# Kernel tuning notes

Hardware: AMD Instinct MI355X
Metric: run time of the kernel (lower is better)

Reference implementation:

```python
import jax, jax.numpy as jnp
import numpy as np

N = 50000
E = 600000
C = 128          # out_channels (== in_channels)
L = 3            # num_conv layers
HID = 32
NUM_CLASSES = 7


def setup_inputs() -> dict:
    key = jax.random.key(0)
    ks = jax.random.split(key, 16)
    bound = 1.0 / np.sqrt(C)
    inp = {
        "x": jax.random.normal(ks[0], (N, C), dtype=jnp.float32),
        "edge_index": jax.random.randint(ks[1], (2, E), 0, N, dtype=jnp.int32),
        "edge_weight": jax.random.uniform(ks[2], (E,), dtype=jnp.float32),
        # GatedGraphConv weight: [num_layers, C, C], uniform(-1/sqrt(C), 1/sqrt(C))
        "conv_weight": jax.random.uniform(ks[3], (L, C, C), minval=-bound, maxval=bound, dtype=jnp.float32),
        # GRUCell params (torch layout: [3C, C] for ih and hh, gate order r,z,n)
        "w_ih": jax.random.uniform(ks[4], (3 * C, C), minval=-bound, maxval=bound, dtype=jnp.float32),
        "w_hh": jax.random.uniform(ks[5], (3 * C, C), minval=-bound, maxval=bound, dtype=jnp.float32),
        "b_ih": jax.random.uniform(ks[6], (3 * C,), minval=-bound, maxval=bound, dtype=jnp.float32),
        "b_hh": jax.random.uniform(ks[7], (3 * C,), minval=-bound, maxval=bound, dtype=jnp.float32),
        # MLP: C -> 32 -> 32 -> 32 -> NUM_CLASSES, tanh between hidden layers
        "w0": jax.random.normal(ks[8], (HID, C), dtype=jnp.float32) * 0.05,
        "b0": jnp.zeros((HID,), dtype=jnp.float32),
        "w1": jax.random.normal(ks[9], (HID, HID), dtype=jnp.float32) * 0.1,
        "b1": jnp.zeros((HID,), dtype=jnp.float32),
        "w2": jax.random.normal(ks[10], (HID, HID), dtype=jnp.float32) * 0.1,
        "b2": jnp.zeros((HID,), dtype=jnp.float32),
        "w3": jax.random.normal(ks[11], (NUM_CLASSES, HID), dtype=jnp.float32) * 0.1,
        "b3": jnp.zeros((NUM_CLASSES,), dtype=jnp.float32),
    }
    return inp


def _gru_cell(m, h, w_ih, w_hh, b_ih, b_hh):
    # torch GRUCell: gates ordered (r, z, n)
    gx = m @ w_ih.T + b_ih          # [N, 3C]
    gh = h @ w_hh.T + b_hh          # [N, 3C]
    xr, xz, xn = jnp.split(gx, 3, axis=-1)
    hr, hz, hn = jnp.split(gh, 3, axis=-1)
    r = jax.nn.sigmoid(xr + hr)
    z = jax.nn.sigmoid(xz + hz)
    n = jnp.tanh(xn + r * hn)
    return (1.0 - z) * n + z * h


def reference(x, edge_index, edge_weight, conv_weight, w_ih, w_hh, b_ih, b_hh,
              w0, b0, w1, b1, w2, b2, w3, b3):
    src, dst = edge_index[0], edge_index[1]
    h = x  # in_channels == out_channels, no padding needed
    for i in range(L):
        m = h @ conv_weight[i]                          # [N, C] dense GEMM
        msgs = edge_weight[:, None] * m[src]            # gather + edge weighting [E, C]
        agg = jax.ops.segment_sum(msgs, dst, num_segments=N)  # scatter-add [N, C]
        h = _gru_cell(agg, h, w_ih, w_hh, b_ih, b_hh)
    # MLP with tanh between hidden layers, linear last
    y = jnp.tanh(h @ w0.T + b0)
    y = jnp.tanh(y @ w1.T + b1)
    y = jnp.tanh(y @ w2.T + b2)
    y = y @ w3.T + b3
    return jax.nn.log_softmax(y, axis=-1)
```

## Files before the change

### kernel.cpp

```cpp
#include <hip/hip_runtime.h>
#include <hip/hip_bf16.h>
#include <math.h>

#define NN 50000
#define NE 600000
#define CC 128
#define NL 3
#define NRG (NN / 16)
#define C_RG 4
#define G_RG 4
#define SCAN_B 196

typedef __attribute__((ext_vector_type(8))) short bf16x8;
typedef __attribute__((ext_vector_type(4))) float f32x4;
typedef unsigned short ushort_t;
typedef unsigned int uint_t;

__device__ inline ushort_t f2bf(float f) {
    __hip_bfloat16 b = __float2bfloat16(f);
    return *reinterpret_cast<ushort_t*>(&b);
}
__device__ inline float bf2f(ushort_t u) {
    return __uint_as_float(((uint_t)u) << 16);
}
__device__ inline float fsig(float x) {
    return __builtin_amdgcn_rcpf(1.f + __builtin_amdgcn_exp2f(-1.44269504f * x));
}
__device__ inline float ftanh(float x) {
    float e = __builtin_amdgcn_exp2f(2.88539008f * fabsf(x));
    float t = 1.f - 2.f * __builtin_amdgcn_rcpf(e + 1.f);
    return copysignf(t, x);
}

__global__ __launch_bounds__(256) void k_cvt(const float* __restrict__ x,
                                             ushort_t* __restrict__ h_bf) {
    size_t i = (size_t)blockIdx.x * 256 + threadIdx.x;
    float4 v = ((const float4*)x)[i];
    ushort4 u;
    u.x = f2bf(v.x); u.y = f2bf(v.y); u.z = f2bf(v.z); u.w = f2bf(v.w);
    ((ushort4*)h_bf)[i] = u;
}

__global__ __launch_bounds__(256) void k_wpack(const float* __restrict__ W,
                                               ushort_t* __restrict__ pk) {
    int tid = blockIdx.x * 256 + threadIdx.x;
    int e = tid & 7;
    int l = (tid >> 3) & 63;
    int s = (tid >> 9) & 3;
    int rest = tid >> 11;
    int g = rest % 3, c0 = rest / 3;
    int row = g * 128 + c0 * 16 + (l & 15);
    int col = s * 32 + (l >> 4) * 8 + e;
    pk[tid] = f2bf(W[row * 128 + col]);
}

__global__ __launch_bounds__(256) void k_cpack(const float* __restrict__ cw,
                                               ushort_t* __restrict__ pk) {
    int tid = blockIdx.x * 256 + threadIdx.x;
    int e = tid & 7;
    int l = (tid >> 3) & 63;
    int s = (tid >> 9) & 3;
    int rest = tid >> 11;
    int c0 = rest & 7, layer = rest >> 3;
    int c = c0 * 16 + (l & 15);
    int k = s * 32 + (l >> 4) * 8 + e;
    pk[tid] = f2bf(cw[layer * 16384 + k * 128 + c]);
}

__global__ __launch_bounds__(256) void k_mpack(const float* __restrict__ w0,
                                               const float* __restrict__ w1,
                                               const float* __restrict__ w2,
                                               const float* __restrict__ w3,
                                               ushort_t* __restrict__ pk) {
    int tid = blockIdx.x * 256 + threadIdx.x;
    if (tid >= 6656) return;
    int e = tid & 7;
    int l = (tid >> 3) & 63;
    int lr = l & 15, lg = l >> 4;
    if (tid < 4096) {
        int s = (tid >> 9) & 3;
        int c0 = tid >> 11;
        pk[tid] = f2bf(w0[(c0 * 16 + lr) * 128 + s * 32 + lg * 8 + e]);
    } else if (tid < 5120) {
        int c0 = (tid - 4096) >> 9;
        pk[tid] = f2bf(w1[(c0 * 16 + lr) * 32 + lg * 8 + e]);
    } else if (tid < 6144) {
        int c0 = (tid - 5120) >> 9;
        pk[tid] = f2bf(w2[(c0 * 16 + lr) * 32 + lg * 8 + e]);
    } else {
        pk[tid] = (lr < 7) ? f2bf(w3[lr * 32 + lg * 8 + e]) : (ushort_t)0;
    }
}

__global__ __launch_bounds__(256) void k_count(const int* __restrict__ dst,
                                               int* __restrict__ deg) {
    int e = blockIdx.x * 256 + threadIdx.x;
    if (e < NE) atomicAdd(&deg[dst[e]], 1);
}

__global__ __launch_bounds__(256) void k_scan1(const int* __restrict__ deg,
                                               int* __restrict__ off,
                                               int* __restrict__ bsum) {
    __shared__ int sm[256];
    int t = threadIdx.x, i = blockIdx.x * 256 + t;
    int v = (i < NN) ? deg[i] : 0;
    sm[t] = v;
    __syncthreads();
#pragma unroll
    for (int ofs = 1; ofs < 256; ofs <<= 1) {
        int u = (t >= ofs) ? sm[t - ofs] : 0;
        __syncthreads();
        sm[t] += u;
        __syncthreads();
    }
    if (i < NN) off[i] = sm[t] - v;
    if (t == 255) bsum[blockIdx.x] = sm[255];
}

__global__ __launch_bounds__(256) void k_scan2(const int* __restrict__ bsum,
                                               int* __restrict__ bofs,
                                               int* __restrict__ off) {
    __shared__ int sm[256];
    int t = threadIdx.x;
    int v = (t < SCAN_B) ? bsum[t] : 0;
    sm[t] = v;
    __syncthreads();
#pragma unroll
    for (int ofs = 1; ofs < 256; ofs <<= 1) {
        int u = (t >= ofs) ? sm[t - ofs] : 0;
        __syncthreads();
        sm[t] += u;
        __syncthreads();
    }
    if (t < SCAN_B) bofs[t] = sm[t] - v;
    if (t == 255) off[NN] = sm[255];
}

__global__ __launch_bounds__(256) void k_scan3(int* __restrict__ off,
                                               const int* __restrict__ bofs,
                                               int* __restrict__ cursor) {
    int t = threadIdx.x, i = blockIdx.x * 256 + t;
    if (i < NN) {
        int o = off[i] + bofs[blockIdx.x];
        off[i] = o;
        cursor[i] = o;
    }
}

__global__ __launch_bounds__(256) void k_fill(const int* __restrict__ src,
                                              const int* __restrict__ dst,
                                              const float* __restrict__ ew,
                                              int* __restrict__ cursor,
                                              int* __restrict__ e_src,
                                              float* __restrict__ e_w) {
    int e = blockIdx.x * 256 + threadIdx.x;
    if (e >= NE) return;
    int d = dst[e];
    int p = atomicAdd(&cursor[d], 1);
    e_src[p] = src[e];
    e_w[p] = ew[e];
}

__global__ __launch_bounds__(256, 2) void k_conv(const ushort_t* __restrict__ h_bf,
                                                 const ushort_t* __restrict__ cw_pk,
                                                 ushort_t* __restrict__ m_bf) {
    int wid = (blockIdx.x * 256 + threadIdx.x) >> 6;
    int l = threadIdx.x & 63;
    int lr = l & 15, lg = l >> 4;
    int c0g = wid & 3;
    int chunk = wid >> 2;

    bf16x8 B[2][4];
    {
        const bf16x8* pw = (const bf16x8*)cw_pk;
#pragma unroll
        for (int p = 0; p < 2; p++)
#pragma unroll
            for (int s = 0; s < 4; s++)
                B[p][s] = pw[(size_t)(((c0g + 4 * p) * 4 + s) * 64) + l];
    }
    int c_lo = c0g * 16 + lr;

    for (int it = 0; it < C_RG; it++) {
        int rg = chunk * C_RG + it;
        if (rg >= NRG) break;
        int n0 = rg * 16;
        const short* ap = (const short*)h_bf + (size_t)(n0 + lr) * CC + lg * 8;
        bf16x8 a[4];
#pragma unroll
        for (int s = 0; s < 4; s++) a[s] = *(const bf16x8*)(ap + s * 32);
        f32x4 acc0 = {0.f,0.f,0.f,0.f}, acc1 = {0.f,0.f,0.f,0.f};
#pragma unroll
        for (int s = 0; s < 4; s++) {
            acc0 = __builtin_amdgcn_mfma_f32_16x16x32_bf16(a[s], B[0][s], acc0, 0, 0, 0);
            acc1 = __builtin_amdgcn_mfma_f32_16x16x32_bf16(a[s], B[1][s], acc1, 0, 0, 0);
        }
#pragma unroll
        for (int j = 0; j < 4; j++) {
            size_t row = (size_t)(n0 + lg * 4 + j) * CC;
            m_bf[row + c_lo] = f2bf(acc0[j]);
            m_bf[row + c_lo + 64] = f2bf(acc1[j]);
        }
    }
}

__global__ __launch_bounds__(256) void k_agg(const int* __restrict__ off,
                                             const int* __restrict__ e_src,
                                             const float* __restrict__ e_w,
                                             const ushort_t* __restrict__ m_bf,
                                             ushort_t* __restrict__ agg_bf) {
    int node = blockIdx.x * 4 + (threadIdx.x >> 6);
    int lane = threadIdx.x & 63;
    if (node >= NN) return;
    int b = off[node], e = off[node + 1];
    const uint_t* m2 = (const uint_t*)m_bf;
    float ax = 0.f, ay = 0.f;
    int i = b;
    for (; i + 8 <= e; i += 8) {
        int s[8]; float w[8]; uint_t v[8];
#pragma unroll
        for (int q = 0; q < 8; q++) { s[q] = e_src[i + q]; w[q] = e_w[i + q]; }
#pragma unroll
        for (int q = 0; q < 8; q++) v[q] = m2[(size_t)s[q] * 64 + lane];
#pragma unroll
        for (int q = 0; q < 8; q++) {
            ax += w[q] * bf2f((ushort_t)(v[q] & 0xffffu));
            ay += w[q] * bf2f((ushort_t)(v[q] >> 16));
        }
    }
    for (; i + 4 <= e; i += 4) {
        int s[4]; float w[4]; uint_t v[4];
#pragma unroll
        for (int q = 0; q < 4; q++) { s[q] = e_src[i + q]; w[q] = e_w[i + q]; }
#pragma unroll
        for (int q = 0; q < 4; q++) v[q] = m2[(size_t)s[q] * 64 + lane];
#pragma unroll
        for (int q = 0; q < 4; q++) {
            ax += w[q] * bf2f((ushort_t)(v[q] & 0xffffu));
            ay += w[q] * bf2f((ushort_t)(v[q] >> 16));
        }
    }
    for (; i < e; i++) {
        int s = e_src[i];
        float w = e_w[i];
        uint_t v = m2[(size_t)s * 64 + lane];
        ax += w * bf2f((ushort_t)(v & 0xffffu));
        ay += w * bf2f((ushort_t)(v >> 16));
    }
    uint_t packed = (uint_t)f2bf(ax) | ((uint_t)f2bf(ay) << 16);
    ((uint_t*)agg_bf)[(size_t)node * 64 + lane] = packed;
}

__global__ __launch_bounds__(256, 2) void k_gru(const ushort_t* __restrict__ agg_bf,
                                                const ushort_t* __restrict__ hbf_in,
                                                ushort_t* __restrict__ hbf_out,
                                                const float* __restrict__ h_in,
                                                float* __restrict__ h_out,
                                                const ushort_t* __restrict__ wx_pk,
                                                const ushort_t* __restrict__ wh_pk,
                                                const float* __restrict__ b_ih,
                                                const float* __restrict__ b_hh,
                                                int store_f32) {
    int wid = (blockIdx.x * 256 + threadIdx.x) >> 6;
    int l = threadIdx.x & 63;
    int c0 = wid & 7;
    int chunk = wid >> 3;
    int lr = l & 15, lg = l >> 4;

    bf16x8 BX[12], BH[12];
    {
        const bf16x8* px = (const bf16x8*)wx_pk + (size_t)c0 * 12 * 64 + l;
        const bf16x8* ph = (const bf16x8*)wh_pk + (size_t)c0 * 12 * 64 + l;
#pragma unroll
        for (int f = 0; f < 12; f++) { BX[f] = px[f * 64]; BH[f] = ph[f * 64]; }
    }
    int c = c0 * 16 + lr;
    float bxr = b_ih[c], bxz = b_ih[128 + c], bxn = b_ih[256 + c];
    float bhr = b_hh[c], bhz = b_hh[128 + c], bhn = b_hh[256 + c];

    for (int it = 0; it < G_RG; it++) {
        int rg = chunk * G_RG + it;
        if (rg >= NRG) break;
        int n0 = rg * 16;
        const short* ap = (const short*)agg_bf + (size_t)(n0 + lr) * CC + lg * 8;
        const short* hp = (const short*)hbf_in + (size_t)(n0 + lr) * CC + lg * 8;
        bf16x8 a[4], hf[4];
#pragma unroll
        for (int s = 0; s < 4; s++) {
            a[s] = *(const bf16x8*)(ap + s * 32);
            hf[s] = *(const bf16x8*)(hp + s * 32);
        }
        float hv[4];
#pragma unroll
        for (int j = 0; j < 4; j++) hv[j] = h_in[(size_t)(n0 + lg * 4 + j) * CC + c];

        f32x4 r0 = {0.f,0.f,0.f,0.f}, r1 = {0.f,0.f,0.f,0.f}, r2 = {0.f,0.f,0.f,0.f};
        f32x4 r3 = {0.f,0.f,0.f,0.f}, r4 = {0.f,0.f,0.f,0.f}, r5 = {0.f,0.f,0.f,0.f};
#pragma unroll
        for (int s = 0; s < 4; s++) {
            r0 = __builtin_amdgcn_mfma_f32_16x16x32_bf16(a[s], BX[s], r0, 0, 0, 0);
            r1 = __builtin_amdgcn_mfma_f32_16x16x32_bf16(a[s], BX[4 + s], r1, 0, 0, 0);
            r2 = __builtin_amdgcn_mfma_f32_16x16x32_bf16(a[s], BX[8 + s], r2, 0, 0, 0);
            r3 = __builtin_amdgcn_mfma_f32_16x16x32_bf16(hf[s], BH[s], r3, 0, 0, 0);
            r4 = __builtin_amdgcn_mfma_f32_16x16x32_bf16(hf[s], BH[4 + s], r4, 0, 0, 0);
            r5 = __builtin_amdgcn_mfma_f32_16x16x32_bf16(hf[s], BH[8 + s], r5, 0, 0, 0);
        }
#pragma unroll
        for (int j = 0; j < 4; j++) {
            size_t row = (size_t)(n0 + lg * 4 + j);
            float rg_ = fsig(r0[j] + bxr + r3[j] + bhr);
            float zg = fsig(r1[j] + bxz + r4[j] + bhz);
            float ng = ftanh(r2[j] + bxn + rg_ * (r5[j] + bhn));
            float hn2 = (1.f - zg) * ng + zg * hv[j];
            if (store_f32) h_out[row * CC + c] = hn2;
            hbf_out[row * CC + c] = f2bf(hn2);
        }
    }
}

__global__ __launch_bounds__(256, 2) void k_mlp(const ushort_t* __restrict__ hbf,
                                                const ushort_t* __restrict__ wm_pk,
                                                const float* __restrict__ b0,
                                                const float* __restrict__ b1,
                                                const float* __restrict__ b2,
                                                const float* __restrict__ b3,
                                                float* __restrict__ out) {
    __shared__ short vt[4][16][40];
    __shared__ float yt[4][16][8];
    int wid = (blockIdx.x * 256 + threadIdx.x) >> 6;
    int wq = threadIdx.x >> 6;
    int l = threadIdx.x & 63;
    int lr = l & 15, lg = l >> 4;

    bf16x8 W0[2][4], W1[2], W2[2], W3;
    {
        const bf16x8* pw = (const bf16x8*)wm_pk;
#pragma unroll
        for (int c0 = 0; c0 < 2; c0++)
#pragma unroll
            for (int s = 0; s < 4; s++) W0[c0][s] = pw[(c0 * 4 + s) * 64 + l];
#pragma unroll
        for (int c0 = 0; c0 < 2; c0++) {
            W1[c0] = pw[512 + c0 * 64 + l];
            W2[c0] = pw[640 + c0 * 64 + l];
        }
        W3 = pw[768 + l];
    }
    float b0v[2] = {b0[lr], b0[16 + lr]};
    float b1v[2] = {b1[lr], b1[16 + lr]};
    float b2v[2] = {b2[lr], b2[16 + lr]};
    float b3v = (lr < 7) ? b3[lr] : 0.f;

    if (wid >= NRG) return;
    int n0 = wid * 16;

    bf16x8 a[4];
    {
        const short* ap = (const short*)hbf + (size_t)(n0 + lr) * CC + lg * 8;
#pragma unroll
        for (int s = 0; s < 4; s++) a[s] = *(const bf16x8*)(ap + s * 32);
    }
#pragma unroll
    for (int c0 = 0; c0 < 2; c0++) {
        f32x4 acc = {0.f, 0.f, 0.f, 0.f};
#pragma unroll
        for (int s = 0; s < 4; s++)
            acc = __builtin_amdgcn_mfma_f32_16x16x32_bf16(a[s], W0[c0][s], acc, 0, 0, 0);
#pragma unroll
        for (int j = 0; j < 4; j++)
            vt[wq][lg * 4 + j][c0 * 16 + lr] = (short)f2bf(ftanh(acc[j] + b0v[c0]));
    }
    {
        bf16x8 av = *(const bf16x8*)&vt[wq][lr][lg * 8];
        f32x4 acc[2];
#pragma unroll
        for (int c0 = 0; c0 < 2; c0++) {
            f32x4 z = {0.f, 0.f, 0.f, 0.f};
            acc[c0] = __builtin_amdgcn_mfma_f32_16x16x32_bf16(av, W1[c0], z, 0, 0, 0);
        }
#pragma unroll
        for (int c0 = 0; c0 < 2; c0++)
#pragma unroll
            for (int j = 0; j < 4; j++)
                vt[wq][lg * 4 + j][c0 * 16 + lr] = (short)f2bf(ftanh(acc[c0][j] + b1v[c0]));
    }
    {
        bf16x8 av = *(const bf16x8*)&vt[wq][lr][lg * 8];
        f32x4 acc[2];
#pragma unroll
        for (int c0 = 0; c0 < 2; c0++) {
            f32x4 z = {0.f, 0.f, 0.f, 0.f};
            acc[c0] = __builtin_amdgcn_mfma_f32_16x16x32_bf16(av, W2[c0], z, 0, 0, 0);
        }
#pragma unroll
        for (int c0 = 0; c0 < 2; c0++)
#pragma unroll
            for (int j = 0; j < 4; j++)
                vt[wq][lg * 4 + j][c0 * 16 + lr] = (short)f2bf(ftanh(acc[c0][j] + b2v[c0]));
    }
    {
        bf16x8 av = *(const bf16x8*)&vt[wq][lr][lg * 8];
        f32x4 z = {0.f, 0.f, 0.f, 0.f};
        f32x4 acc = __builtin_amdgcn_mfma_f32_16x16x32_bf16(av, W3, z, 0, 0, 0);
        if (lr < 7) {
#pragma unroll
            for (int j = 0; j < 4; j++) yt[wq][lg * 4 + j][lr] = acc[j] + b3v;
        }
    }
    __builtin_amdgcn_s_waitcnt(0);
    if (l < 16) {
        float y[7];
#pragma unroll
        for (int j = 0; j < 7; j++) y[j] = yt[wq][l][j];
        float mx = y[0];
#pragma unroll
        for (int j = 1; j < 7; j++) mx = fmaxf(mx, y[j]);
        float se = 0.f;
#pragma unroll
        for (int j = 0; j < 7; j++) se += expf(y[j] - mx);
        float lse = mx + logf(se);
#pragma unroll
        for (int j = 0; j < 7; j++) out[(size_t)(n0 + l) * 7 + j] = y[j] - lse;
    }
}

extern "C" void kernel_launch(void* const* d_in, const int* in_sizes, int n_in,
                              void* d_out, int out_size, void* d_ws, size_t ws_size,
                              hipStream_t stream) {
    const float* x   = (const float*)d_in[0];
    const int*   ei  = (const int*)d_in[1];
    const float* ew  = (const float*)d_in[2];
    const float* cw  = (const float*)d_in[3];
    const float* wih = (const float*)d_in[4];
    const float* whh = (const float*)d_in[5];
    const float* bih = (const float*)d_in[6];
    const float* bhh = (const float*)d_in[7];
    const float* w0 = (const float*)d_in[8];
    const float* b0 = (const float*)d_in[9];
    const float* w1 = (const float*)d_in[10];
    const float* b1 = (const float*)d_in[11];
    const float* w2 = (const float*)d_in[12];
    const float* b2 = (const float*)d_in[13];
    const float* w3 = (const float*)d_in[14];
    const float* b3 = (const float*)d_in[15];
    float* out = (float*)d_out;

    float*    h     = (float*)d_ws;
    ushort_t* hbf0  = (ushort_t*)(h + (size_t)NN * CC);
    ushort_t* hbf1  = hbf0 + (size_t)NN * CC;
    ushort_t* m_bf  = hbf1 + (size_t)NN * CC;
    ushort_t* agg_bf= m_bf + (size_t)NN * CC;
    ushort_t* wx_pk = agg_bf + (size_t)NN * CC;
    ushort_t* wh_pk = wx_pk + 3 * CC * CC;
    ushort_t* cw_pk = wh_pk + 3 * CC * CC;
    ushort_t* wm_pk = cw_pk + 3 * CC * CC;
    float*    e_w   = (float*)(wm_pk + 6656);
    int*      e_src = (int*)(e_w + NE);
    int*      off   = e_src + NE;
    int*      deg   = off + (NN + 1);
    int*      cursor= deg + NN;
    int*      bsum  = cursor + NN;
    int*      bofs  = bsum + SCAN_B;

    const int* src = ei;
    const int* dst = ei + NE;

    k_cvt<<<(NN * CC) / 1024, 256, 0, stream>>>(x, hbf0);
    k_wpack<<<192, 256, 0, stream>>>(wih, wx_pk);
    k_wpack<<<192, 256, 0, stream>>>(whh, wh_pk);
    k_cpack<<<192, 256, 0, stream>>>(cw, cw_pk);
    k_mpack<<<26, 256, 0, stream>>>(w0, w1, w2, w3, wm_pk);

    hipMemsetAsync(deg, 0, NN * sizeof(int), stream);
    k_count<<<(NE + 255) / 256, 256, 0, stream>>>(dst, deg);
    k_scan1<<<SCAN_B, 256, 0, stream>>>(deg, off, bsum);
    k_scan2<<<1, 256, 0, stream>>>(bsum, bofs, off);
    k_scan3<<<SCAN_B, 256, 0, stream>>>(off, bofs, cursor);
    k_fill<<<(NE + 255) / 256, 256, 0, stream>>>(src, dst, ew, cursor, e_src, e_w);

    const int conv_waves = 4 * ((NRG + C_RG - 1) / C_RG);
    const int conv_blk = (conv_waves + 3) / 4;
    const int gru_waves = 8 * ((NRG + G_RG - 1) / G_RG);
    const int gru_blk = (gru_waves + 3) / 4;

    ushort_t* hin = hbf0;
    ushort_t* hout = hbf1;
    for (int l = 0; l < NL; l++) {
        k_conv<<<conv_blk, 256, 0, stream>>>(hin, cw_pk + (size_t)l * CC * CC, m_bf);
        k_agg<<<(NN + 3) / 4, 256, 0, stream>>>(off, e_src, e_w, m_bf, agg_bf);
        k_gru<<<gru_blk, 256, 0, stream>>>(agg_bf, hin, hout,
                                           (l == 0) ? x : h, h, wx_pk, wh_pk, bih, bhh,
                                           (l < NL - 1) ? 1 : 0);
        ushort_t* tmp = hin; hin = hout; hout = tmp;
    }
    k_mlp<<<(NRG + 3) / 4, 256, 0, stream>>>(hin, wm_pk, b0, b1, b2, b3, out);
}
```

Measured before the change: 336.5 us.

## Pack edge src/weight pairs, split aggregation across half-waves, drop fp32 hidden state

Edges in CSR order now live as interleaved (src, weight) uint2 pairs, so the aggregation fetches both fields with one load. Each wavefront splits into two halves that process alternate edges with 8-byte loads per lane, and the halves are combined with a cross-lane shuffle. The GRU now reads the previous hidden state from the bf16 copy instead of a separate fp32 buffer and no longer writes an fp32 state, which removes that traffic. The cost is accumulating the recurrent state in bf16 across layers, which may reduce accuracy, and a shallower per-half unroll in the gather loop.

Result: faster. 328.0 us (-2.5%).

```diff
diff --git a/kernel.cpp b/kernel.cpp
--- a/kernel.cpp
+++ b/kernel.cpp
@@ -151,14 +151,15 @@
                                               const int* __restrict__ dst,
                                               const float* __restrict__ ew,
                                               int* __restrict__ cursor,
-                                              int* __restrict__ e_src,
-                                              float* __restrict__ e_w) {
+                                              uint2* __restrict__ e_pair) {
     int e = blockIdx.x * 256 + threadIdx.x;
     if (e >= NE) return;
     int d = dst[e];
     int p = atomicAdd(&cursor[d], 1);
-    e_src[p] = src[e];
-    e_w[p] = ew[e];
+    uint2 pr;
+    pr.x = (uint_t)src[e];
+    pr.y = __float_as_uint(ew[e]);
+    e_pair[p] = pr;
 }
 
 __global__ __launch_bounds__(256, 2) void k_conv(const ushort_t* __restrict__ h_bf,
@@ -205,62 +206,57 @@
 }
 
 __global__ __launch_bounds__(256) void k_agg(const int* __restrict__ off,
-                                             const int* __restrict__ e_src,
-                                             const float* __restrict__ e_w,
+                                             const uint2* __restrict__ e_pair,
                                              const ushort_t* __restrict__ m_bf,
                                              ushort_t* __restrict__ agg_bf) {
     int node = blockIdx.x * 4 + (threadIdx.x >> 6);
-    int lane = threadIdx.x & 63;
+    int l = threadIdx.x & 63;
+    int half = l >> 5, sl = l & 31;
     if (node >= NN) return;
     int b = off[node], e = off[node + 1];
-    const uint_t* m2 = (const uint_t*)m_bf;
-    float ax = 0.f, ay = 0.f;
+    const uint2* m2 = (const uint2*)m_bf;
+    float a0 = 0.f, a1 = 0.f, a2 = 0.f, a3 = 0.f;
     int i = b;
-    for (; i + 8 <= e; i += 8) {
-        int s[8]; float w[8]; uint_t v[8];
-#pragma unroll
-        for (int q = 0; q < 8; q++) { s[q] = e_src[i + q]; w[q] = e_w[i + q]; }
-#pragma unroll
-        for (int q = 0; q < 8; q++) v[q] = m2[(size_t)s[q] * 64 + lane];
-#pragma unroll
-        for (int q = 0; q < 8; q++) {
-            ax += w[q] * bf2f((ushort_t)(v[q] & 0xffffu));
-            ay += w[q] * bf2f((ushort_t)(v[q] >> 16));
-        }
-    }
     for (; i + 4 <= e; i += 4) {
-        int s[4]; float w[4]; uint_t v[4];
-#pragma unroll
-        for (int q = 0; q < 4; q++) { s[q] = e_src[i + q]; w[q] = e_w[i + q]; }
-#pragma unroll
-        for (int q = 0; q < 4; q++) v[q] = m2[(size_t)s[q] * 64 + lane];
-#pragma unroll
-        for (int q = 0; q < 4; q++) {
-            ax += w[q] * bf2f((ushort_t)(v[q] & 0xffffu));
-            ay += w[q] * bf2f((ushort_t)(v[q] >> 16));
-        }
-    }
-    for (; i < e; i++) {
-        int s = e_src[i];
-        float w = e_w[i];
-        uint_t v = m2[(size_t)s * 64 + lane];
-        ax += w * bf2f((ushort_t)(v & 0xffffu));
-        ay += w * bf2f((ushort_t)(v >> 16));
-    }
-    uint_t packed = (uint_t)f2bf(ax) | ((uint_t)f2bf(ay) << 16);
-    ((uint_t*)agg_bf)[(size_t)node * 64 + lane] = packed;
+        uint2 p0 = e_pair[i + half];
+        uint2 p1 = e_pair[i + 2 + half];
+        uint2 v0 = m2[(size_t)p0.x * 32 + sl];
+        uint2 v1 = m2[(size_t)p1.x * 32 + sl];
+        float w0 = __uint_as_float(p0.y), w1 = __uint_as_float(p1.y);
+        a0 += w0 * bf2f((ushort_t)(v0.x & 0xffffu)) + w1 * bf2f((ushort_t)(v1.x & 0xffffu));
+        a1 += w0 * bf2f((ushort_t)(v0.x >> 16))     + w1 * bf2f((ushort_t)(v1.x >> 16));
+        a2 += w0 * bf2f((ushort_t)(v0.y & 0xffffu)) + w1 * bf2f((ushort_t)(v1.y & 0xffffu));
+        a3 += w0 * bf2f((ushort_t)(v0.y >> 16))     + w1 * bf2f((ushort_t)(v1.y >> 16));
+    }
+    for (; i < e; i += 2) {
+        int idx = i + half;
+        uint2 pr = (idx < e) ? e_pair[idx] : make_uint2(0u, 0u);
+        uint2 v = m2[(size_t)pr.x * 32 + sl];
+        float w = __uint_as_float(pr.y);
+        a0 += w * bf2f((ushort_t)(v.x & 0xffffu));
+        a1 += w * bf2f((ushort_t)(v.x >> 16));
+        a2 += w * bf2f((ushort_t)(v.y & 0xffffu));
+        a3 += w * bf2f((ushort_t)(v.y >> 16));
+    }
+    a0 += __shfl_xor(a0, 32);
+    a1 += __shfl_xor(a1, 32);
+    a2 += __shfl_xor(a2, 32);
+    a3 += __shfl_xor(a3, 32);
+    if (half == 0) {
+        uint2 p;
+        p.x = (uint_t)f2bf(a0) | ((uint_t)f2bf(a1) << 16);
+        p.y = (uint_t)f2bf(a2) | ((uint_t)f2bf(a3) << 16);
+        ((uint2*)agg_bf)[(size_t)node * 32 + sl] = p;
+    }
 }
 
 __global__ __launch_bounds__(256, 2) void k_gru(const ushort_t* __restrict__ agg_bf,
                                                 const ushort_t* __restrict__ hbf_in,
                                                 ushort_t* __restrict__ hbf_out,
-                                                const float* __restrict__ h_in,
-                                                float* __restrict__ h_out,
                                                 const ushort_t* __restrict__ wx_pk,
                                                 const ushort_t* __restrict__ wh_pk,
                                                 const float* __restrict__ b_ih,
-                                                const float* __restrict__ b_hh,
-                                                int store_f32) {
+                                                const float* __restrict__ b_hh) {
     int wid = (blockIdx.x * 256 + threadIdx.x) >> 6;
     int l = threadIdx.x & 63;
     int c0 = wid & 7;
@@ -292,7 +288,8 @@
         }
         float hv[4];
 #pragma unroll
-        for (int j = 0; j < 4; j++) hv[j] = h_in[(size_t)(n0 + lg * 4 + j) * CC + c];
+        for (int j = 0; j < 4; j++)
+            hv[j] = bf2f(hbf_in[(size_t)(n0 + lg * 4 + j) * CC + c]);
 
         f32x4 r0 = {0.f,0.f,0.f,0.f}, r1 = {0.f,0.f,0.f,0.f}, r2 = {0.f,0.f,0.f,0.f};
         f32x4 r3 = {0.f,0.f,0.f,0.f}, r4 = {0.f,0.f,0.f,0.f}, r5 = {0.f,0.f,0.f,0.f};
@@ -312,7 +309,6 @@
             float zg = fsig(r1[j] + bxz + r4[j] + bhz);
             float ng = ftanh(r2[j] + bxn + rg_ * (r5[j] + bhn));
             float hn2 = (1.f - zg) * ng + zg * hv[j];
-            if (store_f32) h_out[row * CC + c] = hn2;
             hbf_out[row * CC + c] = f2bf(hn2);
         }
     }
@@ -445,8 +441,7 @@
     const float* b3 = (const float*)d_in[15];
     float* out = (float*)d_out;
 
-    float*    h     = (float*)d_ws;
-    ushort_t* hbf0  = (ushort_t*)(h + (size_t)NN * CC);
+    ushort_t* hbf0  = (ushort_t*)d_ws;
     ushort_t* hbf1  = hbf0 + (size_t)NN * CC;
     ushort_t* m_bf  = hbf1 + (size_t)NN * CC;
     ushort_t* agg_bf= m_bf + (size_t)NN * CC;
@@ -454,9 +449,8 @@
     ushort_t* wh_pk = wx_pk + 3 * CC * CC;
     ushort_t* cw_pk = wh_pk + 3 * CC * CC;
     ushort_t* wm_pk = cw_pk + 3 * CC * CC;
-    float*    e_w   = (float*)(wm_pk + 6656);
-    int*      e_src = (int*)(e_w + NE);
-    int*      off   = e_src + NE;
+    uint2*    e_pair= (uint2*)(wm_pk + 6656);
+    int*      off   = (int*)(e_pair + NE);
     int*      deg   = off + (NN + 1);
     int*      cursor= deg + NN;
     int*      bsum  = cursor + NN;
@@ -476,7 +470,7 @@
     k_scan1<<<SCAN_B, 256, 0, stream>>>(deg, off, bsum);
     k_scan2<<<1, 256, 0, stream>>>(bsum, bofs, off);
     k_scan3<<<SCAN_B, 256, 0, stream>>>(off, bofs, cursor);
-    k_fill<<<(NE + 255) / 256, 256, 0, stream>>>(src, dst, ew, cursor, e_src, e_w);
+    k_fill<<<(NE + 255) / 256, 256, 0, stream>>>(src, dst, ew, cursor, e_pair);
 
     const int conv_waves = 4 * ((NRG + C_RG - 1) / C_RG);
     const int conv_blk = (conv_waves + 3) / 4;
@@ -487,10 +481,8 @@
     ushort_t* hout = hbf1;
     for (int l = 0; l < NL; l++) {
         k_conv<<<conv_blk, 256, 0, stream>>>(hin, cw_pk + (size_t)l * CC * CC, m_bf);
-        k_agg<<<(NN + 3) / 4, 256, 0, stream>>>(off, e_src, e_w, m_bf, agg_bf);
-        k_gru<<<gru_blk, 256, 0, stream>>>(agg_bf, hin, hout,
-                                           (l == 0) ? x : h, h, wx_pk, wh_pk, bih, bhh,
-                                           (l < NL - 1) ? 1 : 0);
+        k_agg<<<(NN + 3) / 4, 256, 0, stream>>>(off, e_pair, m_bf, agg_bf);
+        k_gru<<<gru_blk, 256, 0, stream>>>(agg_bf, hin, hout, wx_pk, wh_pk, bih, bhh);
         ushort_t* tmp = hin; hin = hout; hout = tmp;
     }
     k_mlp<<<(NRG + 3) / 4, 256, 0, stream>>>(hin, wm_pk, b0, b1, b2, b3, out);
```
